# Kernel optimization log

Measured on AMD Instinct MI355X. Metric: run time of the kernel, lower is better.

Reference implementation:

```python
import jax, jax.numpy as jnp
import numpy as np

B, S, D, H = 2, 2048, 1024, 16
DH = D // H  # depth per head = 64


def setup_inputs() -> dict:
    key = jax.random.key(0)
    ks = jax.random.split(key, 5)
    sc = 0.02
    return {
        "x": jax.random.normal(ks[0], (B, S, D), dtype=jnp.float32),
        "Wq": jax.random.normal(ks[1], (D, D), dtype=jnp.float32) * sc,
        "bq": jnp.zeros((D,), dtype=jnp.float32),
        "Wk": jax.random.normal(ks[2], (D, D), dtype=jnp.float32) * sc,
        "bk": jnp.zeros((D,), dtype=jnp.float32),
        "Wv": jax.random.normal(ks[3], (D, D), dtype=jnp.float32) * sc,
        "bv": jnp.zeros((D,), dtype=jnp.float32),
        "Wo": jax.random.normal(ks[4], (D, D), dtype=jnp.float32) * sc,
        "bo": jnp.zeros((D,), dtype=jnp.float32),
    }


def _split_heads(t):
    # [B,S,D] -> [B,H,S,DH]
    return t.reshape(B, S, H, DH).transpose(0, 2, 1, 3)


def reference(x, Wq, bq, Wk, bk, Wv, bv, Wo, bo):
    q = _split_heads(x @ Wq + bq)
    k = _split_heads(x @ Wk + bk)
    v = _split_heads(x @ Wv + bv)
    scale = 1.0 / jnp.sqrt(jnp.float32(DH))
    logits = jnp.einsum("bhqd,bhkd->bhqk", q, k) * scale  # [B,H,S,S]
    attn = jax.nn.softmax(logits, axis=-1)
    ctx = jnp.einsum("bhqk,bhkd->bhqd", attn, v)
    ctx = ctx.transpose(0, 2, 1, 3).reshape(B, S, D)
    # dropout is identity at inference
    return ctx @ Wo + bo
```

## Files before the change

### kernel.cpp

```cpp
#include <hip/hip_runtime.h>
#include <hip/hip_bf16.h>

#define S_LEN   2048
#define D_MODEL 1024
#define NHEAD   16
#define DHEAD   64
#define M_ROWS  4096
#define BHEADS  32
#define MEG     1048576

typedef __attribute__((ext_vector_type(8)))  short short8;
typedef __attribute__((ext_vector_type(4)))  float f32x4;
typedef __attribute__((ext_vector_type(16))) float f32x16;
typedef __attribute__((ext_vector_type(4)))  unsigned short us4;
typedef __attribute__((ext_vector_type(2)))  unsigned int uint2v;
typedef __attribute__((ext_vector_type(4)))  unsigned int uint4v;

extern "C" __device__ float __ocml_native_exp2_f32(float);

__device__ __forceinline__ unsigned short f2b(float f) {
    unsigned int u = __builtin_bit_cast(unsigned int, f);
    return (unsigned short)((u + 0x7FFFu + ((u >> 16) & 1u)) >> 16);
}

__device__ __forceinline__ unsigned int cvtpk(float lo, float hi) {
    unsigned int r;
    asm("v_cvt_pk_bf16_f32 %0, %1, %2" : "=v"(r) : "v"(lo), "v"(hi));
    return r;
}

__device__ __forceinline__ float b2f(unsigned short b) {
    return __builtin_bit_cast(float, (unsigned int)b << 16);
}

#define GLOAD16(gp, lp) __builtin_amdgcn_global_load_lds(                     \
        (const __attribute__((address_space(1))) void*)(gp),                  \
        (__attribute__((address_space(3))) void*)(lp), 16, 0, 0)

#define STAGE_OFS(lane) ((((lane) & 3) ^ (((lane) >> 3) & 3)) * 8)

__global__ __launch_bounds__(256) void prep(
    const float* __restrict__ x, unsigned short* __restrict__ xb,
    const float* __restrict__ Wq, const float* __restrict__ Wk,
    const float* __restrict__ Wv, const float* __restrict__ Wo,
    unsigned short* __restrict__ Wqt, unsigned short* __restrict__ Wkt,
    unsigned short* __restrict__ Wvt, unsigned short* __restrict__ Wot)
{
    const int z = blockIdx.z;
    const int tx = threadIdx.x, ty = threadIdx.y;
    if (z == 4) {
        const int blk = blockIdx.y * 32 + blockIdx.x;
        const int base = (blk * 256 + ty * 32 + tx) * 4;
        #pragma unroll
        for (int r = 0; r < 4; ++r) {
            const int i = base + r * (M_ROWS * D_MODEL / 4);
            const float4 v = *(const float4*)&x[i];
            us4 o;
            o.x = f2b(v.x); o.y = f2b(v.y); o.z = f2b(v.z); o.w = f2b(v.w);
            *(us4*)&xb[i] = o;
        }
        return;
    }
    __shared__ float tile[32][33];
    const float* W = z == 0 ? Wq : (z == 1 ? Wk : (z == 2 ? Wv : Wo));
    unsigned short* Wt = z == 0 ? Wqt : (z == 1 ? Wkt : (z == 2 ? Wvt : Wot));
    const int n0 = blockIdx.x * 32, k0 = blockIdx.y * 32;
    #pragma unroll
    for (int i = 0; i < 4; ++i)
        tile[ty + i * 8][tx] = W[(size_t)(k0 + ty + i * 8) * D_MODEL + n0 + tx];
    __syncthreads();
    #pragma unroll
    for (int i = 0; i < 4; ++i)
        Wt[(size_t)(n0 + ty + i * 8) * D_MODEL + k0 + tx] = f2b(tile[tx][ty + i * 8]);
}

__global__ __launch_bounds__(256) void gemm_qkv(
    const unsigned short* __restrict__ xb,
    const unsigned short* __restrict__ Wqt, const unsigned short* __restrict__ Wkt,
    const unsigned short* __restrict__ Wvt,
    const float* __restrict__ bq, const float* __restrict__ bk,
    const float* __restrict__ bv,
    unsigned short* __restrict__ Qb, unsigned short* __restrict__ Kb,
    unsigned short* __restrict__ Vt)
{
    __shared__ unsigned short As[2][128][32];
    __shared__ unsigned short Bs[2][128][32];

    const int z = blockIdx.z;
    const unsigned short* Wt = z == 0 ? Wqt : (z == 1 ? Wkt : Wvt);
    const float* bias = z == 0 ? bq : (z == 1 ? bk : bv);

    const int t = threadIdx.x, lane = t & 63, w = t >> 6;
    const int wm = w >> 1, wn = w & 1;
    const int bm = blockIdx.y * 128, bn = blockIdx.x * 128;
    const int lr = lane >> 2, lc = STAGE_OFS(lane);
    const int lm = lane & 15, quad = lane >> 4;
    const int qo = (quad ^ ((lm >> 1) & 3)) * 8;

    f32x4 acc[4][4] = {};

    #pragma unroll
    for (int i = 0; i < 2; ++i) {
        const int c = 2 * w + i;
        GLOAD16(xb + (size_t)(bm + c * 16 + lr) * D_MODEL + lc, &As[0][c * 16][0]);
        GLOAD16(Wt + (size_t)(bn + c * 16 + lr) * D_MODEL + lc, &Bs[0][c * 16][0]);
    }
    __syncthreads();

    for (int it = 0; it < 32; ++it) {
        const int cur = it & 1;
        if (it + 1 < 32) {
            const int kt = (it + 1) * 32;
            #pragma unroll
            for (int i = 0; i < 2; ++i) {
                const int c = 2 * w + i;
                GLOAD16(xb + (size_t)(bm + c * 16 + lr) * D_MODEL + kt + lc,
                        &As[cur ^ 1][c * 16][0]);
                GLOAD16(Wt + (size_t)(bn + c * 16 + lr) * D_MODEL + kt + lc,
                        &Bs[cur ^ 1][c * 16][0]);
            }
        }

        short8 af[4], bfr[4];
        #pragma unroll
        for (int mi = 0; mi < 4; ++mi)
            af[mi] = *(const short8*)&As[cur][wm * 64 + mi * 16 + lm][qo];
        #pragma unroll
        for (int ni = 0; ni < 4; ++ni)
            bfr[ni] = *(const short8*)&Bs[cur][wn * 64 + ni * 16 + lm][qo];
        #pragma unroll
        for (int mi = 0; mi < 4; ++mi)
            #pragma unroll
            for (int ni = 0; ni < 4; ++ni)
                acc[mi][ni] = __builtin_amdgcn_mfma_f32_16x16x32_bf16(
                    af[mi], bfr[ni], acc[mi][ni], 0, 0, 0);

        __syncthreads();
    }

    float bb[4];
    #pragma unroll
    for (int ni = 0; ni < 4; ++ni)
        bb[ni] = bias[bn + wn * 64 + ni * 16 + lm];
    const float scale = (z == 0) ? 0.18033688011112042f : 1.0f;

    if (z < 2) {
        unsigned short* Out = (z == 0) ? Qb : Kb;
        #pragma unroll
        for (int mi = 0; mi < 4; ++mi)
            #pragma unroll
            for (int r = 0; r < 4; ++r) {
                const int row = bm + wm * 64 + mi * 16 + quad * 4 + r;
                const int b = row >> 11, s = row & 2047;
                #pragma unroll
                for (int ni = 0; ni < 4; ++ni) {
                    const int col = bn + wn * 64 + ni * 16 + lm;
                    const int h = col >> 6, d = col & 63;
                    Out[(((size_t)(b * NHEAD + h)) * S_LEN + s) * DHEAD + d] =
                        f2b((acc[mi][ni][r] + bb[ni]) * scale);
                }
            }
    } else {
        #pragma unroll
        for (int mi = 0; mi < 4; ++mi) {
            const int row0 = bm + wm * 64 + mi * 16 + quad * 4;
            const int b = row0 >> 11, s0 = row0 & 2047;
            #pragma unroll
            for (int ni = 0; ni < 4; ++ni) {
                const int col = bn + wn * 64 + ni * 16 + lm;
                const int h = col >> 6, d = col & 63;
                us4 pk;
                pk.x = f2b(acc[mi][ni][0] + bb[ni]);
                pk.y = f2b(acc[mi][ni][1] + bb[ni]);
                pk.z = f2b(acc[mi][ni][2] + bb[ni]);
                pk.w = f2b(acc[mi][ni][3] + bb[ni]);
                *(us4*)&Vt[(((size_t)(b * NHEAD + h)) * DHEAD + d) * S_LEN + s0] = pk;
            }
        }
    }
}

__global__ __launch_bounds__(256) void gemm_out(
    const unsigned short* __restrict__ Ab, const unsigned short* __restrict__ Wot,
    const float* __restrict__ bo, float* __restrict__ out)
{
    __shared__ unsigned short As[2][64][32];
    __shared__ unsigned short Bs[2][128][32];

    const int t = threadIdx.x, lane = t & 63, w = t >> 6;
    const int wm = w & 1, wn = w >> 1;
    const int bm = blockIdx.y * 64, bn = blockIdx.x * 128;
    const int lr = lane >> 2, lc = STAGE_OFS(lane);
    const int lm = lane & 15, quad = lane >> 4;
    const int qo = (quad ^ ((lm >> 1) & 3)) * 8;

    f32x4 acc[2][4] = {};

    GLOAD16(Ab + (size_t)(bm + w * 16 + lr) * D_MODEL + lc, &As[0][w * 16][0]);
    #pragma unroll
    for (int i = 0; i < 2; ++i)
        GLOAD16(Wot + (size_t)(bn + w * 32 + i * 16 + lr) * D_MODEL + lc,
                &Bs[0][w * 32 + i * 16][0]);
    __syncthreads();

    for (int it = 0; it < 32; ++it) {
        const int cur = it & 1;
        if (it + 1 < 32) {
            const int kt = (it + 1) * 32;
            GLOAD16(Ab + (size_t)(bm + w * 16 + lr) * D_MODEL + kt + lc,
                    &As[cur ^ 1][w * 16][0]);
            #pragma unroll
            for (int i = 0; i < 2; ++i)
                GLOAD16(Wot + (size_t)(bn + w * 32 + i * 16 + lr) * D_MODEL + kt + lc,
                        &Bs[cur ^ 1][w * 32 + i * 16][0]);
        }

        short8 af[2], bfr[4];
        #pragma unroll
        for (int mi = 0; mi < 2; ++mi)
            af[mi] = *(const short8*)&As[cur][wm * 32 + mi * 16 + lm][qo];
        #pragma unroll
        for (int ni = 0; ni < 4; ++ni)
            bfr[ni] = *(const short8*)&Bs[cur][wn * 64 + ni * 16 + lm][qo];
        #pragma unroll
        for (int mi = 0; mi < 2; ++mi)
            #pragma unroll
            for (int ni = 0; ni < 4; ++ni)
                acc[mi][ni] = __builtin_amdgcn_mfma_f32_16x16x32_bf16(
                    af[mi], bfr[ni], acc[mi][ni], 0, 0, 0);

        __syncthreads();
    }

    float bb[4];
    #pragma unroll
    for (int ni = 0; ni < 4; ++ni)
        bb[ni] = bo[bn + wn * 64 + ni * 16 + lm];

    #pragma unroll
    for (int mi = 0; mi < 2; ++mi)
        #pragma unroll
        for (int r = 0; r < 4; ++r) {
            const int row = bm + wm * 32 + mi * 16 + quad * 4 + r;
            #pragma unroll
            for (int ni = 0; ni < 4; ++ni) {
                const int col = bn + wn * 64 + ni * 16 + lm;
                out[(size_t)row * D_MODEL + col] = acc[mi][ni][r] + bb[ni];
            }
        }
}

__global__ __launch_bounds__(256, 4) void attn_mfma(
    const unsigned short* __restrict__ Q, const unsigned short* __restrict__ K,
    const unsigned short* __restrict__ V, unsigned short* __restrict__ Cx)
{
    __shared__ __align__(16) unsigned char raw[33280];
    unsigned short (*Qs)[128][32] = (unsigned short (*)[128][32])raw;
    float* Ls = (float*)(raw + 32768);

    const int t = threadIdx.x, lane = t & 63, w = t >> 6;
    const int q5 = lane & 31, hi = lane >> 5;
    const int lr = lane >> 2, lcs = STAGE_OFS(lane);
    const int id  = blockIdx.y * 16 + blockIdx.x;
    const int swz = (id & 7) * 64 + (id >> 3);
    const int q0 = (swz & 15) * 128, bh = swz >> 4;
    const int sw = (q5 >> 1) & 3;
    int sbo[4];
    #pragma unroll
    for (int sb = 0; sb < 4; ++sb) sbo[sb] = (sb ^ sw) * 8;

    const unsigned short* Qh = Q + (size_t)bh * (S_LEN * DHEAD);
    const unsigned short* Kh = K + (size_t)bh * (S_LEN * DHEAD);
    const unsigned short* Vh = V + (size_t)bh * (DHEAD * S_LEN);

    #pragma unroll
    for (int i = 0; i < 2; ++i)
        #pragma unroll
        for (int c = 0; c < 2; ++c)
            GLOAD16(Qh + (size_t)(q0 + w * 32 + c * 16 + lr) * DHEAD + i * 32 + lcs,
                    &Qs[i][w * 32 + c * 16][0]);
    __syncthreads();

    short8 qf[4];
    #pragma unroll
    for (int c = 0; c < 4; ++c)
        qf[c] = *(const short8*)&Qs[c >> 1][w * 32 + q5][sbo[(c & 1) * 2 + hi]];
    __syncthreads();

    #define STAGE_KV(IT, BUF) do {                                            \
        const int kt_ = (IT) * 64;                                            \
        unsigned short* ksb_ = (unsigned short*)(raw + (BUF) * 16384);        \
        unsigned short* vsb_ = ksb_ + 4096;                                   \
        _Pragma("unroll")                                                     \
        for (int i_ = 0; i_ < 2; ++i_) {                                      \
            GLOAD16(Kh + (size_t)(kt_ + w * 16 + lr) * DHEAD + i_ * 32 + lcs, \
                    ksb_ + (i_ * 64 + w * 16) * 32);                          \
            GLOAD16(Vh + (size_t)(w * 16 + lr) * S_LEN + kt_ + i_ * 32 + lcs, \
                    vsb_ + (i_ * 64 + w * 16) * 32);                          \
        }                                                                     \
    } while (0)

    STAGE_KV(0, 0);

    f32x16 acc[2] = {};
    float2 l2a = {0.f, 0.f}, l2b = {0.f, 0.f};

    for (int it = 0; it < 32; ++it) {
        const int cur = it & 1;
        __syncthreads();
        if (it + 1 < 32)
            STAGE_KV(it + 1, cur ^ 1);

        const unsigned short* ks = (const unsigned short*)(raw + cur * 16384);
        const unsigned short* vs = ks + 4096;

        f32x16 sf[2] = {};
        #pragma unroll
        for (int c = 0; c < 4; ++c) {
            #pragma unroll
            for (int mt = 0; mt < 2; ++mt) {
                const short8 kf = *(const short8*)
                    &ks[((c >> 1) * 64 + mt * 32 + q5) * 32 + sbo[(c & 1) * 2 + hi]];
                sf[mt] = __builtin_amdgcn_mfma_f32_32x32x16_bf16(kf, qf[c], sf[mt], 0, 0, 0);
            }
        }

        #pragma unroll
        for (int c = 0; c < 4; ++c) {
            const int mt = c >> 1, pp = c & 1;
            float p[8];
            #pragma unroll
            for (int e = 0; e < 8; ++e)
                p[e] = __ocml_native_exp2_f32(sf[mt][pp * 8 + e]);
            l2a.x += p[0]; l2a.y += p[1]; l2b.x += p[2]; l2b.y += p[3];
            l2a.x += p[4]; l2a.y += p[5]; l2b.x += p[6]; l2b.y += p[7];
            const unsigned int dA = cvtpk(p[0], p[1]);
            const unsigned int dB = cvtpk(p[2], p[3]);
            const unsigned int sA = cvtpk(p[4], p[5]);
            const unsigned int sB = cvtpk(p[6], p[7]);
            const uint2v wA = __builtin_amdgcn_permlane32_swap(dA, sA, false, false);
            const uint2v wB = __builtin_amdgcn_permlane32_swap(dB, sB, false, false);
            uint4v wrds;
            wrds.x = wA.x; wrds.y = wB.x; wrds.z = wA.y; wrds.w = wB.y;
            const short8 pf = __builtin_bit_cast(short8, wrds);
            #pragma unroll
            for (int nt = 0; nt < 2; ++nt) {
                const short8 vf = *(const short8*)
                    &vs[((c >> 1) * 64 + nt * 32 + q5) * 32 + sbo[(c & 1) * 2 + hi]];
                acc[nt] = __builtin_amdgcn_mfma_f32_32x32x16_bf16(pf, vf, acc[nt], 0, 0, 0);
            }
        }
    }
    #undef STAGE_KV

    float l_acc = (l2a.x + l2a.y) + (l2b.x + l2b.y);
    l_acc += __shfl_xor(l_acc, 32);
    if (hi == 0)
        Ls[w * 32 + q5] = l_acc;
    const int b = bh >> 4, h = bh & 15;
    #pragma unroll
    for (int reg = 0; reg < 16; ++reg) {
        const int row = (reg & 3) + 8 * (reg >> 2) + 4 * hi;
        const float inv = 1.f / Ls[w * 32 + row];
        const int q = q0 + w * 32 + row;
        unsigned short* dst = &Cx[((size_t)(b * S_LEN + q)) * D_MODEL + h * 64];
        dst[q5]      = f2b(acc[0][reg] * inv);
        dst[32 + q5] = f2b(acc[1][reg] * inv);
    }
}

extern "C" void kernel_launch(void* const* d_in, const int* in_sizes, int n_in,
                              void* d_out, int out_size, void* d_ws, size_t ws_size,
                              hipStream_t stream)
{
    const float* x  = (const float*)d_in[0];
    const float* Wq = (const float*)d_in[1];
    const float* bq = (const float*)d_in[2];
    const float* Wk = (const float*)d_in[3];
    const float* bk = (const float*)d_in[4];
    const float* Wv = (const float*)d_in[5];
    const float* bv = (const float*)d_in[6];
    const float* Wo = (const float*)d_in[7];
    const float* bo = (const float*)d_in[8];
    float* out = (float*)d_out;

    unsigned short* base = (unsigned short*)d_ws;
    unsigned short* Wot   = base;
    unsigned short* Qb    = base + 1 * MEG;
    unsigned short* Kb    = base + 5 * MEG;
    unsigned short* Vt    = base + 9 * MEG;
    unsigned short* xb    = base + 13 * MEG;
    unsigned short* Wqt   = base + 17 * MEG;
    unsigned short* Wkt   = base + 18 * MEG;
    unsigned short* Wvt   = base + 19 * MEG;
    unsigned short* Cxb   = xb;

    prep<<<dim3(32, 32, 5), dim3(32, 8), 0, stream>>>(
        x, xb, Wq, Wk, Wv, Wo, Wqt, Wkt, Wvt, Wot);

    gemm_qkv<<<dim3(D_MODEL / 128, M_ROWS / 128, 3), dim3(256), 0, stream>>>(
        xb, Wqt, Wkt, Wvt, bq, bk, bv, Qb, Kb, Vt);

    attn_mfma<<<dim3(S_LEN / 128, BHEADS), dim3(256), 0, stream>>>(
        Qb, Kb, Vt, Cxb);

    gemm_out<<<dim3(D_MODEL / 128, M_ROWS / 64), dim3(256), 0, stream>>>(
        Cxb, Wot, bo, out);
}
```

Measured before the change: 197.8 us.

## Software-pipeline QK^T one tile ahead with triple-buffered KV and MFMA row sums

Restructures the attention inner loop so the QK^T MFMA chain for tile it+1 is issued before the softmax/PV work of tile it, using a triple-buffered K/V LDS ring with prefetch two tiles ahead. The softmax denominator is now computed by an extra MFMA against a ones vector instead of scalar adds and a cross-lane shuffle plus LDS reduction. LDS grows to 48KB and occupancy hint drops from 4 to 2 blocks per SIMD group, trading occupancy for intra-wave overlap of exp/VALU work with matrix ops. The row sum is now accumulated from bf16-rounded probabilities, which slightly changes numerics.

```diff
diff --git a/kernel.cpp b/kernel.cpp
--- a/kernel.cpp
+++ b/kernel.cpp
@@ -38,6 +38,9 @@
         (__attribute__((address_space(3))) void*)(lp), 16, 0, 0)
 
 #define STAGE_OFS(lane) ((((lane) & 3) ^ (((lane) >> 3) & 3)) * 8)
+
+#define ZERO16(v) do { _Pragma("unroll")                                      \
+    for (int z_ = 0; z_ < 16; ++z_) (v)[z_] = 0.f; } while (0)
 
 __global__ __launch_bounds__(256) void prep(
     const float* __restrict__ x, unsigned short* __restrict__ xb,
@@ -250,13 +253,12 @@
         }
 }
 
-__global__ __launch_bounds__(256, 4) void attn_mfma(
+__global__ __launch_bounds__(256, 2) void attn_mfma(
     const unsigned short* __restrict__ Q, const unsigned short* __restrict__ K,
     const unsigned short* __restrict__ V, unsigned short* __restrict__ Cx)
 {
-    __shared__ __align__(16) unsigned char raw[33280];
+    __shared__ __align__(16) unsigned char raw[49152];
     unsigned short (*Qs)[128][32] = (unsigned short (*)[128][32])raw;
-    float* Ls = (float*)(raw + 32768);
 
     const int t = threadIdx.x, lane = t & 63, w = t >> 6;
     const int q5 = lane & 31, hi = lane >> 5;
@@ -286,6 +288,10 @@
     for (int c = 0; c < 4; ++c)
         qf[c] = *(const short8*)&Qs[c >> 1][w * 32 + q5][sbo[(c & 1) * 2 + hi]];
     __syncthreads();
+
+    short8 onesf;
+    #pragma unroll
+    for (int j = 0; j < 8; ++j) onesf[j] = (short)0x3F80;
 
     #define STAGE_KV(IT, BUF) do {                                            \
         const int kt_ = (IT) * 64;                                            \
@@ -300,68 +306,85 @@
         }                                                                     \
     } while (0)
 
+    #define QK_CHAIN(IT, SF) do {                                             \
+        const unsigned short* kn_ = (const unsigned short*)                   \
+            (raw + ((IT) % 3) * 16384);                                       \
+        _Pragma("unroll")                                                     \
+        for (int c_ = 0; c_ < 4; ++c_) {                                      \
+            _Pragma("unroll")                                                 \
+            for (int mt_ = 0; mt_ < 2; ++mt_) {                               \
+                const short8 kf_ = *(const short8*)                           \
+                    &kn_[((c_ >> 1) * 64 + mt_ * 32 + q5) * 32                \
+                         + sbo[(c_ & 1) * 2 + hi]];                           \
+                SF[mt_] = __builtin_amdgcn_mfma_f32_32x32x16_bf16(            \
+                    kf_, qf[c_], SF[mt_], 0, 0, 0);                           \
+            }                                                                 \
+        }                                                                     \
+    } while (0)
+
+    f32x16 acc[2];
+    f32x16 acc_l;
+    ZERO16(acc[0]); ZERO16(acc[1]); ZERO16(acc_l);
+    f32x16 sfA[2], sfB[2];
+
     STAGE_KV(0, 0);
-
-    f32x16 acc[2] = {};
-    float2 l2a = {0.f, 0.f}, l2b = {0.f, 0.f};
-
-    for (int it = 0; it < 32; ++it) {
-        const int cur = it & 1;
-        __syncthreads();
-        if (it + 1 < 32)
-            STAGE_KV(it + 1, cur ^ 1);
-
-        const unsigned short* ks = (const unsigned short*)(raw + cur * 16384);
-        const unsigned short* vs = ks + 4096;
-
-        f32x16 sf[2] = {};
-        #pragma unroll
-        for (int c = 0; c < 4; ++c) {
-            #pragma unroll
-            for (int mt = 0; mt < 2; ++mt) {
-                const short8 kf = *(const short8*)
-                    &ks[((c >> 1) * 64 + mt * 32 + q5) * 32 + sbo[(c & 1) * 2 + hi]];
-                sf[mt] = __builtin_amdgcn_mfma_f32_32x32x16_bf16(kf, qf[c], sf[mt], 0, 0, 0);
-            }
-        }
-
-        #pragma unroll
-        for (int c = 0; c < 4; ++c) {
-            const int mt = c >> 1, pp = c & 1;
-            float p[8];
-            #pragma unroll
-            for (int e = 0; e < 8; ++e)
-                p[e] = __ocml_native_exp2_f32(sf[mt][pp * 8 + e]);
-            l2a.x += p[0]; l2a.y += p[1]; l2b.x += p[2]; l2b.y += p[3];
-            l2a.x += p[4]; l2a.y += p[5]; l2b.x += p[6]; l2b.y += p[7];
-            const unsigned int dA = cvtpk(p[0], p[1]);
-            const unsigned int dB = cvtpk(p[2], p[3]);
-            const unsigned int sA = cvtpk(p[4], p[5]);
-            const unsigned int sB = cvtpk(p[6], p[7]);
-            const uint2v wA = __builtin_amdgcn_permlane32_swap(dA, sA, false, false);
-            const uint2v wB = __builtin_amdgcn_permlane32_swap(dB, sB, false, false);
-            uint4v wrds;
-            wrds.x = wA.x; wrds.y = wB.x; wrds.z = wA.y; wrds.w = wB.y;
-            const short8 pf = __builtin_bit_cast(short8, wrds);
-            #pragma unroll
-            for (int nt = 0; nt < 2; ++nt) {
-                const short8 vf = *(const short8*)
-                    &vs[((c >> 1) * 64 + nt * 32 + q5) * 32 + sbo[(c & 1) * 2 + hi]];
-                acc[nt] = __builtin_amdgcn_mfma_f32_32x32x16_bf16(pf, vf, acc[nt], 0, 0, 0);
-            }
-        }
-    }
+    __syncthreads();
+    ZERO16(sfA[0]); ZERO16(sfA[1]);
+    QK_CHAIN(0, sfA);
+    STAGE_KV(1, 1);
+
+    #define REGION(IT, SFC, SFN, DOQK) do {                                   \
+        __syncthreads();                                                      \
+        if ((IT) + 2 < 32) STAGE_KV((IT) + 2, ((IT) + 2) % 3);                \
+        if (DOQK) {                                                           \
+            ZERO16(SFN[0]); ZERO16(SFN[1]);                                   \
+            QK_CHAIN((IT) + 1, SFN);                                          \
+        }                                                                     \
+        const unsigned short* vs_ = (const unsigned short*)                   \
+            (raw + ((IT) % 3) * 16384) + 4096;                                \
+        _Pragma("unroll")                                                     \
+        for (int c = 0; c < 4; ++c) {                                         \
+            const int mt = c >> 1, pp = c & 1;                                \
+            float p[8];                                                       \
+            _Pragma("unroll")                                                 \
+            for (int e = 0; e < 8; ++e)                                       \
+                p[e] = __ocml_native_exp2_f32(SFC[mt][pp * 8 + e]);           \
+            const unsigned int dA = cvtpk(p[0], p[1]);                        \
+            const unsigned int dB = cvtpk(p[2], p[3]);                        \
+            const unsigned int sA = cvtpk(p[4], p[5]);                        \
+            const unsigned int sB = cvtpk(p[6], p[7]);                        \
+            const uint2v wA = __builtin_amdgcn_permlane32_swap(dA, sA, false, false); \
+            const uint2v wB = __builtin_amdgcn_permlane32_swap(dB, sB, false, false); \
+            uint4v wrds;                                                      \
+            wrds.x = wA.x; wrds.y = wB.x; wrds.z = wA.y; wrds.w = wB.y;       \
+            const short8 pf = __builtin_bit_cast(short8, wrds);               \
+            acc_l = __builtin_amdgcn_mfma_f32_32x32x16_bf16(                  \
+                pf, onesf, acc_l, 0, 0, 0);                                   \
+            _Pragma("unroll")                                                 \
+            for (int nt = 0; nt < 2; ++nt) {                                  \
+                const short8 vf = *(const short8*)                            \
+                    &vs_[((c >> 1) * 64 + nt * 32 + q5) * 32                  \
+                         + sbo[(c & 1) * 2 + hi]];                            \
+                acc[nt] = __builtin_amdgcn_mfma_f32_32x32x16_bf16(            \
+                    pf, vf, acc[nt], 0, 0, 0);                                \
+            }                                                                 \
+        }                                                                     \
+    } while (0)
+
+    for (int itp = 0; itp < 16; ++itp) {
+        const int it0 = itp * 2;
+        REGION(it0, sfA, sfB, true);
+        REGION(it0 + 1, sfB, sfA, (it0 + 2) < 32);
+    }
+    #undef REGION
+    #undef QK_CHAIN
     #undef STAGE_KV
 
-    float l_acc = (l2a.x + l2a.y) + (l2b.x + l2b.y);
-    l_acc += __shfl_xor(l_acc, 32);
-    if (hi == 0)
-        Ls[w * 32 + q5] = l_acc;
     const int b = bh >> 4, h = bh & 15;
     #pragma unroll
     for (int reg = 0; reg < 16; ++reg) {
         const int row = (reg & 3) + 8 * (reg >> 2) + 4 * hi;
-        const float inv = 1.f / Ls[w * 32 + row];
+        const float inv = 1.f / acc_l[reg];
         const int q = q0 + w * 32 + row;
         unsigned short* dst = &Cx[((size_t)(b * S_LEN + q)) * D_MODEL + h * 64];
         dst[q5]      = f2b(acc[0][reg] * inv);
```

Result: faster. 193.5 us (-2.2%).

## Double KV tile to 128, compute row sums via MFMA, add setprio scheduling

Applied to the files above, without the earlier changes.

The attention kernel now stages 128 keys per iteration into a 64KB double-buffered LDS region, which halves the number of loop iterations and barriers, and drops occupancy to two blocks per CU. The softmax denominator is no longer built from scalar adds plus a shuffle and LDS round trip. Instead an extra MFMA multiplies the probability fragment by a ones vector, so the row sums land in the same layout as the output accumulator. s_setprio hints wrap the MFMA sections to encourage overlap between waves. The trade-offs are lower occupancy, more LDS, and one extra MFMA per probability chunk, and the sums are now taken from bf16-rounded probabilities.

```diff
diff --git a/kernel.cpp b/kernel.cpp
--- a/kernel.cpp
+++ b/kernel.cpp
@@ -38,6 +38,9 @@
         (__attribute__((address_space(3))) void*)(lp), 16, 0, 0)
 
 #define STAGE_OFS(lane) ((((lane) & 3) ^ (((lane) >> 3) & 3)) * 8)
+
+#define ZERO16(v) do { _Pragma("unroll")                                      \
+    for (int z_ = 0; z_ < 16; ++z_) (v)[z_] = 0.f; } while (0)
 
 __global__ __launch_bounds__(256) void prep(
     const float* __restrict__ x, unsigned short* __restrict__ xb,
@@ -250,13 +253,12 @@
         }
 }
 
-__global__ __launch_bounds__(256, 4) void attn_mfma(
+__global__ __launch_bounds__(256, 2) void attn_mfma(
     const unsigned short* __restrict__ Q, const unsigned short* __restrict__ K,
     const unsigned short* __restrict__ V, unsigned short* __restrict__ Cx)
 {
-    __shared__ __align__(16) unsigned char raw[33280];
+    __shared__ __align__(16) unsigned char raw[65536];
     unsigned short (*Qs)[128][32] = (unsigned short (*)[128][32])raw;
-    float* Ls = (float*)(raw + 32768);
 
     const int t = threadIdx.x, lane = t & 63, w = t >> 6;
     const int q5 = lane & 31, hi = lane >> 5;
@@ -287,81 +289,92 @@
         qf[c] = *(const short8*)&Qs[c >> 1][w * 32 + q5][sbo[(c & 1) * 2 + hi]];
     __syncthreads();
 
+    short8 onesf;
+    #pragma unroll
+    for (int j = 0; j < 8; ++j) onesf[j] = (short)0x3F80;
+
     #define STAGE_KV(IT, BUF) do {                                            \
-        const int kt_ = (IT) * 64;                                            \
-        unsigned short* ksb_ = (unsigned short*)(raw + (BUF) * 16384);        \
-        unsigned short* vsb_ = ksb_ + 4096;                                   \
+        const int kt_ = (IT) * 128;                                           \
+        unsigned short* ksb_ = (unsigned short*)(raw + (BUF) * 32768);        \
+        unsigned short* vsb_ = ksb_ + 8192;                                   \
         _Pragma("unroll")                                                     \
-        for (int i_ = 0; i_ < 2; ++i_) {                                      \
-            GLOAD16(Kh + (size_t)(kt_ + w * 16 + lr) * DHEAD + i_ * 32 + lcs, \
-                    ksb_ + (i_ * 64 + w * 16) * 32);                          \
+        for (int c_ = 0; c_ < 2; ++c_)                                        \
+            _Pragma("unroll")                                                 \
+            for (int i_ = 0; i_ < 2; ++i_)                                    \
+                GLOAD16(Kh + (size_t)(kt_ + c_ * 64 + w * 16 + lr) * DHEAD    \
+                            + i_ * 32 + lcs,                                  \
+                        ksb_ + (i_ * 128 + c_ * 64 + w * 16) * 32);           \
+        _Pragma("unroll")                                                     \
+        for (int i_ = 0; i_ < 4; ++i_)                                        \
             GLOAD16(Vh + (size_t)(w * 16 + lr) * S_LEN + kt_ + i_ * 32 + lcs, \
                     vsb_ + (i_ * 64 + w * 16) * 32);                          \
-        }                                                                     \
     } while (0)
 
+    f32x16 acc[2];
+    f32x16 acc_l;
+    ZERO16(acc[0]); ZERO16(acc[1]); ZERO16(acc_l);
+
     STAGE_KV(0, 0);
 
-    f32x16 acc[2] = {};
-    float2 l2a = {0.f, 0.f}, l2b = {0.f, 0.f};
-
-    for (int it = 0; it < 32; ++it) {
+    for (int it = 0; it < 16; ++it) {
         const int cur = it & 1;
         __syncthreads();
-        if (it + 1 < 32)
+        if (it + 1 < 16)
             STAGE_KV(it + 1, cur ^ 1);
 
-        const unsigned short* ks = (const unsigned short*)(raw + cur * 16384);
-        const unsigned short* vs = ks + 4096;
-
-        f32x16 sf[2] = {};
-        #pragma unroll
-        for (int c = 0; c < 4; ++c) {
-            #pragma unroll
-            for (int mt = 0; mt < 2; ++mt) {
+        const unsigned short* ks = (const unsigned short*)(raw + cur * 32768);
+        const unsigned short* vs = ks + 8192;
+
+        #pragma unroll
+        for (int mt = 0; mt < 4; ++mt) {
+            f32x16 sf;
+            ZERO16(sf);
+            __builtin_amdgcn_s_setprio(1);
+            #pragma unroll
+            for (int c = 0; c < 4; ++c) {
                 const short8 kf = *(const short8*)
-                    &ks[((c >> 1) * 64 + mt * 32 + q5) * 32 + sbo[(c & 1) * 2 + hi]];
-                sf[mt] = __builtin_amdgcn_mfma_f32_32x32x16_bf16(kf, qf[c], sf[mt], 0, 0, 0);
-            }
-        }
-
-        #pragma unroll
-        for (int c = 0; c < 4; ++c) {
-            const int mt = c >> 1, pp = c & 1;
-            float p[8];
-            #pragma unroll
-            for (int e = 0; e < 8; ++e)
-                p[e] = __ocml_native_exp2_f32(sf[mt][pp * 8 + e]);
-            l2a.x += p[0]; l2a.y += p[1]; l2b.x += p[2]; l2b.y += p[3];
-            l2a.x += p[4]; l2a.y += p[5]; l2b.x += p[6]; l2b.y += p[7];
-            const unsigned int dA = cvtpk(p[0], p[1]);
-            const unsigned int dB = cvtpk(p[2], p[3]);
-            const unsigned int sA = cvtpk(p[4], p[5]);
-            const unsigned int sB = cvtpk(p[6], p[7]);
-            const uint2v wA = __builtin_amdgcn_permlane32_swap(dA, sA, false, false);
-            const uint2v wB = __builtin_amdgcn_permlane32_swap(dB, sB, false, false);
-            uint4v wrds;
-            wrds.x = wA.x; wrds.y = wB.x; wrds.z = wA.y; wrds.w = wB.y;
-            const short8 pf = __builtin_bit_cast(short8, wrds);
-            #pragma unroll
-            for (int nt = 0; nt < 2; ++nt) {
-                const short8 vf = *(const short8*)
-                    &vs[((c >> 1) * 64 + nt * 32 + q5) * 32 + sbo[(c & 1) * 2 + hi]];
-                acc[nt] = __builtin_amdgcn_mfma_f32_32x32x16_bf16(pf, vf, acc[nt], 0, 0, 0);
+                    &ks[((c >> 1) * 128 + mt * 32 + q5) * 32
+                        + sbo[(c & 1) * 2 + hi]];
+                sf = __builtin_amdgcn_mfma_f32_32x32x16_bf16(kf, qf[c], sf, 0, 0, 0);
+            }
+            __builtin_amdgcn_s_setprio(0);
+
+            #pragma unroll
+            for (int pp = 0; pp < 2; ++pp) {
+                float p[8];
+                #pragma unroll
+                for (int e = 0; e < 8; ++e)
+                    p[e] = __ocml_native_exp2_f32(sf[pp * 8 + e]);
+                const unsigned int dA = cvtpk(p[0], p[1]);
+                const unsigned int dB = cvtpk(p[2], p[3]);
+                const unsigned int sA = cvtpk(p[4], p[5]);
+                const unsigned int sB = cvtpk(p[6], p[7]);
+                const uint2v wA = __builtin_amdgcn_permlane32_swap(dA, sA, false, false);
+                const uint2v wB = __builtin_amdgcn_permlane32_swap(dB, sB, false, false);
+                uint4v wrds;
+                wrds.x = wA.x; wrds.y = wB.x; wrds.z = wA.y; wrds.w = wB.y;
+                const short8 pf = __builtin_bit_cast(short8, wrds);
+                __builtin_amdgcn_s_setprio(1);
+                acc_l = __builtin_amdgcn_mfma_f32_32x32x16_bf16(
+                    pf, onesf, acc_l, 0, 0, 0);
+                #pragma unroll
+                for (int nt = 0; nt < 2; ++nt) {
+                    const short8 vf = *(const short8*)
+                        &vs[(mt * 64 + nt * 32 + q5) * 32 + sbo[pp * 2 + hi]];
+                    acc[nt] = __builtin_amdgcn_mfma_f32_32x32x16_bf16(
+                        pf, vf, acc[nt], 0, 0, 0);
+                }
+                __builtin_amdgcn_s_setprio(0);
             }
         }
     }
     #undef STAGE_KV
 
-    float l_acc = (l2a.x + l2a.y) + (l2b.x + l2b.y);
-    l_acc += __shfl_xor(l_acc, 32);
-    if (hi == 0)
-        Ls[w * 32 + q5] = l_acc;
     const int b = bh >> 4, h = bh & 15;
     #pragma unroll
     for (int reg = 0; reg < 16; ++reg) {
         const int row = (reg & 3) + 8 * (reg >> 2) + 4 * hi;
-        const float inv = 1.f / Ls[w * 32 + row];
+        const float inv = 1.f / acc_l[reg];
         const int q = q0 + w * 32 + row;
         unsigned short* dst = &Cx[((size_t)(b * S_LEN + q)) * D_MODEL + h * 64];
         dst[q5]      = f2b(acc[0][reg] * inv);
```

New measurement: 195.3 us. About the same (-1.3%).
